# Optimization experiments

Measured on AMD Instinct MI355X. Metric: run time of the kernel, lower is better.

Reference implementation:

```python
import jax, jax.numpy as jnp
import numpy as np

B, S, H, NH = 4, 1024, 1024, 16
DH = H // NH  # 64


def setup_inputs() -> dict:
    key = jax.random.key(0)
    ks = jax.random.split(key, 12)
    f = lambda i, shape: jax.random.normal(ks[i], shape, jnp.float32) * 0.02
    inp = {
        "v": f(0, (B, S, H)),
        "k": f(1, (B, S, H)),
        "q": f(2, (B, S, H)),
        "s": f(3, (B, S, H)),
    }
    # padding-style key mask: last quarter of positions masked (True = masked)
    inp["mask"] = jnp.broadcast_to((jnp.arange(S) >= (3 * S) // 4)[None, None, None, :], (B, 1, 1, S))
    # weights stored as [in, out] so y = x @ W + b (== torch Linear with W = weight.T)
    for i, n in enumerate(["v", "k", "q", "m", "c", "ac"]):
        inp["W" + n] = f(4 + i, (H, H))
        inp["b" + n] = jnp.zeros((H,), jnp.float32)
    inp["Wcc"] = f(10, (H, 1)); inp["bcc"] = jnp.zeros((1,), jnp.float32)
    inp["Wcp"] = f(11, (H, 1)); inp["bcp"] = jnp.zeros((1,), jnp.float32)
    return inp


def reference(v, k, q, s, mask, Wv, bv, Wk, bk, Wq, bq, Wm, bm, Wc, bc, Wac, bac, Wcc, bcc, Wcp, bcp):
    # --- context gating path ---
    g_k = jnp.mean(s, axis=1, keepdims=True) @ Wac + bac          # [B,1,H]  (AdaptiveAvgPool2d((1,None)) + lin_ac)
    merge_p = (s @ Wc + bc) + (g_k @ Wcc + bcc)                   # [B,S,H] + [B,1,1]
    context_p = jax.nn.sigmoid(merge_p)                            # [B,S,H]
    context_gp = jax.nn.sigmoid(context_p @ Wcp + bcp)            # [B,S,1]

    # --- multi-head attention (dropout is identity in eval mode) ---
    def heads(x, W, b):
        return (x @ W + b).reshape(B, S, NH, DH).transpose(0, 2, 1, 3)  # [B,NH,S,DH]

    qh, kh, vh = heads(q, Wq, bq), heads(k, Wk, bk), heads(v, Wv, bv)
    scores = jnp.einsum("bhqd,bhkd->bhqk", qh, kh) / jnp.sqrt(jnp.float32(DH))
    scores = jnp.where(mask, jnp.float32(-1e9), scores)
    att = jax.nn.softmax(scores, axis=-1)
    atted = jnp.einsum("bhqk,bhkd->bhqd", att, vh)
    atted = atted.transpose(0, 2, 1, 3).reshape(B, S, H)
    atted = atted @ Wm + bm                                        # linear_merge
    return context_gp * atted + atted
```

## Files before the change

### kernel.cpp

```cpp
#include <hip/hip_runtime.h>
#include <stdint.h>

#define BB 4
#define SS 1024
#define HH 1024
#define NHEAD 16
#define DHEAD 64

typedef __attribute__((ext_vector_type(8))) short bf16x8;
typedef __attribute__((ext_vector_type(4))) float f32x4;

__device__ __forceinline__ unsigned short f2bf(float f) {
    union { float f; unsigned int u; } v; v.f = f;
    unsigned int r = v.u + 0x7fffu + ((v.u >> 16) & 1u);
    return (unsigned short)(r >> 16);
}
__device__ __forceinline__ float bf2f(unsigned short u) {
    union { float f; unsigned int u; } v; v.u = ((unsigned int)u) << 16;
    return v.f;
}

typedef const __attribute__((address_space(1))) unsigned int* gas_ptr;
typedef __attribute__((address_space(3))) unsigned int* las_ptr;
__device__ __forceinline__ void g2l16(const void* g, void* l) {
    __builtin_amdgcn_global_load_lds((gas_ptr)g, (las_ptr)l, 16, 0, 0);
}

__device__ __forceinline__ int aslot(int row, int c) {
    return row * 64 + ((c ^ (row & 7)) * 8);
}
#define AS_ROW(l) ((l) >> 3)
#define AS_COL(l) (((((l) & 7) ^ ((l) >> 3))) * 8)

__global__ __launch_bounds__(256) void k_prep(
    const float* __restrict__ W0, const float* __restrict__ W1,
    const float* __restrict__ W2, const float* __restrict__ W3,
    const float* __restrict__ W4,
    unsigned short* __restrict__ T0, unsigned short* __restrict__ T1,
    unsigned short* __restrict__ T2, unsigned short* __restrict__ T3,
    unsigned short* __restrict__ T4,
    const float* __restrict__ v, const float* __restrict__ k,
    const float* __restrict__ q, const float* __restrict__ s,
    unsigned short* __restrict__ Av, unsigned short* __restrict__ Ak,
    unsigned short* __restrict__ Aq, unsigned short* __restrict__ Ac,
    float* __restrict__ mpart,
    const float* __restrict__ Wac, const float* __restrict__ Wcc,
    float* __restrict__ u)
{
    int bid = blockIdx.x;
    int tid = threadIdx.x;
    if (bid < 1280) {
        int w = bid >> 8, rem = bid & 255;
        int kt = rem & 15, nt = rem >> 4;
        const float* W; unsigned short* T;
        switch (w) {
            case 0: W = W0; T = T0; break;
            case 1: W = W1; T = T1; break;
            case 2: W = W2; T = T2; break;
            case 3: W = W3; T = T3; break;
            default: W = W4; T = T4; break;
        }
        float scl = (w == 2) ? 0.125f : 1.0f;
        __shared__ unsigned short t[64][68];
        int k0 = kt * 64, n0 = nt * 64;
        int rb = tid >> 4;
        int c4 = (tid & 15) * 4;
#pragma unroll
        for (int i = 0; i < 4; i++) {
            int r = rb + i * 16;
            float4 wv = *(const float4*)&W[(size_t)(k0 + r) * HH + n0 + c4];
            t[c4 + 0][r] = f2bf(wv.x * scl);
            t[c4 + 1][r] = f2bf(wv.y * scl);
            t[c4 + 2][r] = f2bf(wv.z * scl);
            t[c4 + 3][r] = f2bf(wv.w * scl);
        }
        __syncthreads();
#pragma unroll
        for (int i = 0; i < 4; i++) {
            int r = rb + i * 16;
            ushort4 o;
            o.x = t[r][c4 + 0]; o.y = t[r][c4 + 1]; o.z = t[r][c4 + 2]; o.w = t[r][c4 + 3];
            *(ushort4*)&T[(size_t)(n0 + r) * HH + k0 + c4] = o;
        }
    } else if (bid < 9472) {
        int idx = bid - 1280;
        int tno = idx >> 11, blk = idx & 2047;
        const float* src; unsigned short* dst;
        switch (tno) {
            case 0: src = v; dst = Av; break;
            case 1: src = k; dst = Ak; break;
            case 2: src = q; dst = Aq; break;
            default: src = s; dst = Ac; break;
        }
        size_t i0 = ((size_t)blk * 256 + tid) * 8;
        float4 a = *(const float4*)&src[i0];
        float4 b = *(const float4*)&src[i0 + 4];
        bf16x8 o;
        o[0] = (short)f2bf(a.x); o[1] = (short)f2bf(a.y); o[2] = (short)f2bf(a.z); o[3] = (short)f2bf(a.w);
        o[4] = (short)f2bf(b.x); o[5] = (short)f2bf(b.y); o[6] = (short)f2bf(b.z); o[7] = (short)f2bf(b.w);
        *(bf16x8*)&dst[i0] = o;
    } else if (bid < 9728) {
        int idx = bid - 9472;
        int hc = idx & 3, b = (idx >> 2) & 3, g = idx >> 4;
        int h = hc * 256 + tid;
        const float* p = s + (size_t)b * SS * HH + (size_t)g * 64 * HH + h;
        float acc = 0.f;
        for (int i = 0; i < 64; i++) acc += p[(size_t)i * HH];
        mpart[(size_t)(b * 16 + g) * HH + h] = acc;
    } else {
        int idx = bid - 9728;
        int row = idx * 8 + (tid >> 5);
        int l32 = tid & 31;
        const float* wr = Wac + (size_t)row * HH;
        float acc = 0.f;
#pragma unroll
        for (int e = 0; e < 32; e++) {
            int h = l32 + e * 32;
            acc += wr[h] * Wcc[h];
        }
#pragma unroll
        for (int m = 1; m <= 16; m <<= 1) acc += __shfl_xor(acc, m, 64);
        if (l32 == 0) u[row] = acc;
    }
}

__global__ __launch_bounds__(256) void k_gemm4(
    const unsigned short* A0, const unsigned short* A1, const unsigned short* A2, const unsigned short* A3,
    const unsigned short* B0, const unsigned short* B1, const unsigned short* B2, const unsigned short* B3,
    const float* b0, const float* b1, const float* b2, const float* b3,
    unsigned short* D0, unsigned short* D1, unsigned short* D2, unsigned short* D3,
    const float* __restrict__ mpart, const float* __restrict__ u,
    const float* __restrict__ bac, const float* __restrict__ Wcc,
    const float* __restrict__ bcc)
{
    __shared__ unsigned short As[128 * 64];
    __shared__ unsigned short Bs[128 * 64];
    int f = blockIdx.x;
    int xcd = f & 7, j = f >> 3;
    int mp = xcd * 4 + (j >> 5);
    int z = (j >> 3) & 3;
    int n = j & 7;
    const unsigned short* A; const unsigned short* Bt; const float* bias; unsigned short* D; int mode; float bsc = 1.f;
    switch (z) {
        case 0: A = A0; Bt = B0; bias = b0; D = D0; mode = 3; break;
        case 1: A = A1; Bt = B1; bias = b1; D = D1; mode = 0; break;
        case 2: A = A2; Bt = B2; bias = b2; D = D2; mode = 0; bsc = 0.125f; break;
        default: A = A3; Bt = B3; bias = b3; D = D3; mode = 1; break;
    }
    int gm = mp * 128, gn = n * 128;
    int tid = threadIdx.x;
    int lane = tid & 63, wave = tid >> 6;
    int wm = (wave >> 1) * 64, wn = (wave & 1) * 64;
    int quad = lane >> 4, mcol = lane & 15;
    int lrow = lane >> 3;
    int gcol = ((lane & 7) ^ lrow) * 8;

    f32x4 acc[4][4];
#pragma unroll
    for (int i = 0; i < 4; i++)
#pragma unroll
        for (int jj = 0; jj < 4; jj++) acc[i][jj] = (f32x4){0.f, 0.f, 0.f, 0.f};

    for (int kk = 0; kk < 1024; kk += 64) {
#pragma unroll
        for (int i = 0; i < 4; i++) {
            int r0 = (wave * 4 + i) * 8;
            g2l16(&A[(size_t)(gm + r0 + lrow) * 1024 + kk + gcol], &As[r0 * 64]);
            g2l16(&Bt[(size_t)(gn + r0 + lrow) * 1024 + kk + gcol], &Bs[r0 * 64]);
        }
        __syncthreads();
#pragma unroll
        for (int kh = 0; kh < 2; kh++) {
            bf16x8 a[4], b[4];
#pragma unroll
            for (int i = 0; i < 4; i++) {
                int row = wm + i * 16 + mcol;
                int ch = (kh * 4 + quad) ^ (mcol & 7);
                a[i] = *(bf16x8*)&As[row * 64 + ch * 8];
            }
#pragma unroll
            for (int jj = 0; jj < 4; jj++) {
                int row = wn + jj * 16 + mcol;
                int ch = (kh * 4 + quad) ^ (mcol & 7);
                b[jj] = *(bf16x8*)&Bs[row * 64 + ch * 8];
            }
#pragma unroll
            for (int i = 0; i < 4; i++)
#pragma unroll
                for (int jj = 0; jj < 4; jj++)
                    acc[i][jj] = __builtin_amdgcn_mfma_f32_16x16x32_bf16(a[i], b[jj], acc[i][jj], 0, 0, 0);
        }
        __syncthreads();
    }

    float ccv = 0.f;
    if (mode == 1) {
        int b_ = gm >> 10;
        float sb = 0.f;
#pragma unroll
        for (int jj2 = 0; jj2 < 4; jj2++) {
            int h = tid + jj2 * 256;
            float cs = 0.f;
#pragma unroll
            for (int g = 0; g < 16; g++) cs += mpart[(size_t)(b_ * 16 + g) * HH + h];
            sb += cs * u[h] + bac[h] * Wcc[h] * 1024.0f;
        }
        float* red = (float*)As;
        red[tid] = sb; __syncthreads();
        for (int st = 128; st; st >>= 1) { if (tid < st) red[tid] += red[tid + st]; __syncthreads(); }
        ccv = red[0] * (1.0f / 1024.0f) + bcc[0];
    }
#pragma unroll
    for (int i = 0; i < 4; i++) {
        int row0 = gm + wm + i * 16 + quad * 4;
#pragma unroll
        for (int jj = 0; jj < 4; jj++) {
            int col = gn + wn + jj * 16 + mcol;
            float bv = bias[col] * bsc;
            if (mode == 3) {
                int b_ = row0 >> 10, tok0 = row0 & 1023;
                int h = col >> 6, d = col & 63;
                ushort4 o;
                o.x = f2bf(acc[i][jj][0] + bv);
                o.y = f2bf(acc[i][jj][1] + bv);
                o.z = f2bf(acc[i][jj][2] + bv);
                o.w = f2bf(acc[i][jj][3] + bv);
                *(ushort4*)&((unsigned short*)D)[((size_t)(b_ * 16 + h) * 64 + d) * 1024 + tok0] = o;
            } else {
#pragma unroll
                for (int r = 0; r < 4; r++) {
                    float vv = acc[i][jj][r] + bv;
                    int rr = row0 + r;
                    if (mode == 0) {
                        D[(size_t)rr * 1024 + col] = f2bf(vv);
                    } else {
                        vv = vv + ccv;
                        vv = 1.f / (1.f + __expf(-vv));
                        D[(size_t)rr * 1024 + col] = f2bf(vv);
                    }
                }
            }
        }
    }
}

__global__ __launch_bounds__(512) void k_gemmf(
    const unsigned short* __restrict__ A, const unsigned short* __restrict__ Bt,
    const float* __restrict__ bias, float* __restrict__ D, const float* __restrict__ gp)
{
    __shared__ unsigned short As[128 * 64];
    __shared__ unsigned short Bs[128 * 64];
    int f = blockIdx.x;
    int xcd = f & 7, j = f >> 3;
    int mp = xcd * 4 + (j >> 3);
    int n = j & 7;
    int gm = mp * 128, gn = n * 128;
    int tid = threadIdx.x;
    int lane = tid & 63, wave = tid >> 6;
    int wm = (wave >> 2) * 64, wn = (wave & 3) * 32;
    int quad = lane >> 4, mcol = lane & 15;
    int lrow = lane >> 3;
    int gcol = ((lane & 7) ^ lrow) * 8;

    f32x4 acc[4][2];
#pragma unroll
    for (int i = 0; i < 4; i++)
#pragma unroll
        for (int jj = 0; jj < 2; jj++) acc[i][jj] = (f32x4){0.f, 0.f, 0.f, 0.f};

    for (int kk = 0; kk < 1024; kk += 64) {
#pragma unroll
        for (int i = 0; i < 2; i++) {
            int r0 = (wave * 2 + i) * 8;
            g2l16(&A[(size_t)(gm + r0 + lrow) * 1024 + kk + gcol], &As[r0 * 64]);
            g2l16(&Bt[(size_t)(gn + r0 + lrow) * 1024 + kk + gcol], &Bs[r0 * 64]);
        }
        __syncthreads();
#pragma unroll
        for (int kh = 0; kh < 2; kh++) {
            bf16x8 a[4], b[2];
#pragma unroll
            for (int i = 0; i < 4; i++) {
                int row = wm + i * 16 + mcol;
                int ch = (kh * 4 + quad) ^ (mcol & 7);
                a[i] = *(bf16x8*)&As[row * 64 + ch * 8];
            }
#pragma unroll
            for (int jj = 0; jj < 2; jj++) {
                int row = wn + jj * 16 + mcol;
                int ch = (kh * 4 + quad) ^ (mcol & 7);
                b[jj] = *(bf16x8*)&Bs[row * 64 + ch * 8];
            }
#pragma unroll
            for (int i = 0; i < 4; i++)
#pragma unroll
                for (int jj = 0; jj < 2; jj++)
                    acc[i][jj] = __builtin_amdgcn_mfma_f32_16x16x32_bf16(a[i], b[jj], acc[i][jj], 0, 0, 0);
        }
        __syncthreads();
    }

#pragma unroll
    for (int i = 0; i < 4; i++) {
        int row0 = gm + wm + i * 16 + quad * 4;
#pragma unroll
        for (int jj = 0; jj < 2; jj++) {
            int col = gn + wn + jj * 16 + mcol;
            float bv = bias[col];
#pragma unroll
            for (int r = 0; r < 4; r++) {
                int rr = row0 + r;
                D[(size_t)rr * 1024 + col] = (acc[i][jj][r] + bv) * (1.f + gp[rr]);
            }
        }
    }
}

__global__ __launch_bounds__(256) void k_attnctx(
    const unsigned short* __restrict__ Pq,
    const unsigned short* __restrict__ Pk,
    const unsigned short* __restrict__ Pvt,
    unsigned short* __restrict__ atted,
    const unsigned short* __restrict__ Pc,
    const float* __restrict__ Wcp, const float* __restrict__ bcp,
    float* __restrict__ gp)
{
    int bid = blockIdx.x;
    int tid = threadIdx.x;
    int lane = tid & 63, wave = tid >> 6;

    if (bid >= 1024) {
        int rowbase = (bid - 1024) * 16 + wave * 4;
        float w[16];
#pragma unroll
        for (int e = 0; e < 4; e++) {
            float4 wv = *(const float4*)&Wcp[lane * 16 + e * 4];
            w[e * 4 + 0] = wv.x; w[e * 4 + 1] = wv.y; w[e * 4 + 2] = wv.z; w[e * 4 + 3] = wv.w;
        }
        float bcpv = bcp[0];
#pragma unroll
        for (int r = 0; r < 4; r++) {
            int row = rowbase + r;
            bf16x8 u0 = *(const bf16x8*)&Pc[(size_t)row * HH + lane * 16];
            bf16x8 u1 = *(const bf16x8*)&Pc[(size_t)row * HH + lane * 16 + 8];
            float sum = 0.f;
#pragma unroll
            for (int e = 0; e < 8; e++) sum += bf2f((unsigned short)u0[e]) * w[e];
#pragma unroll
            for (int e = 0; e < 8; e++) sum += bf2f((unsigned short)u1[e]) * w[8 + e];
#pragma unroll
            for (int m = 1; m <= 32; m <<= 1) sum += __shfl_xor(sum, m, 64);
            if (lane == 0) gp[row] = 1.f / (1.f + __expf(-(sum + bcpv)));
        }
        return;
    }

    __shared__ unsigned short Qs[64 * 64];
    __shared__ unsigned short Ks[2][64 * 64];
    __shared__ unsigned short Vt[2][64 * 64];
    __shared__ unsigned short Ps[64 * 76];

    int qt = bid & 15;
    int bh = bid >> 4;
    int b = bh >> 4, h = bh & 15;
    int quad = lane >> 4, mcol = lane & 15;
    int srow = AS_ROW(lane), scol = AS_COL(lane);

    size_t base_q = ((size_t)b * SS + qt * 64) * HH + h * 64;
    size_t base_vt = (size_t)(b * 16 + h) * 64 * 1024;

    {
        int r0 = wave * 16;
        g2l16(&Pq[base_q + (size_t)(r0 + srow) * HH + scol], &Qs[r0 * 64]);
        g2l16(&Pq[base_q + (size_t)(r0 + 8 + srow) * HH + scol], &Qs[(r0 + 8) * 64]);
        size_t base_k = (size_t)b * SS * HH + h * 64;
        g2l16(&Pk[base_k + (size_t)(r0 + srow) * HH + scol], &Ks[0][r0 * 64]);
        g2l16(&Pk[base_k + (size_t)(r0 + 8 + srow) * HH + scol], &Ks[0][(r0 + 8) * 64]);
        g2l16(&Pvt[base_vt + (size_t)(r0 + srow) * 1024 + scol], &Vt[0][r0 * 64]);
        g2l16(&Pvt[base_vt + (size_t)(r0 + 8 + srow) * 1024 + scol], &Vt[0][(r0 + 8) * 64]);
    }
    __syncthreads();
    int qrow = wave * 16 + mcol;
    bf16x8 bq0 = *(bf16x8*)&Qs[aslot(qrow, quad)];
    bf16x8 bq1 = *(bf16x8*)&Qs[aslot(qrow, quad + 4)];

    float lsum = 0.f;
    f32x4 acc_o[4];
#pragma unroll
    for (int dg = 0; dg < 4; dg++) acc_o[dg] = (f32x4){0.f, 0.f, 0.f, 0.f};

    for (int kt = 0; kt < 12; kt++) {
        int cur = kt & 1;
        if (kt < 11) {
            int r0 = wave * 16;
            size_t base_k = ((size_t)b * SS + (kt + 1) * 64) * HH + h * 64;
            g2l16(&Pk[base_k + (size_t)(r0 + srow) * HH + scol], &Ks[cur ^ 1][r0 * 64]);
            g2l16(&Pk[base_k + (size_t)(r0 + 8 + srow) * HH + scol], &Ks[cur ^ 1][(r0 + 8) * 64]);
            g2l16(&Pvt[base_vt + (size_t)(r0 + srow) * 1024 + (kt + 1) * 64 + scol], &Vt[cur ^ 1][r0 * 64]);
            g2l16(&Pvt[base_vt + (size_t)(r0 + 8 + srow) * 1024 + (kt + 1) * 64 + scol], &Vt[cur ^ 1][(r0 + 8) * 64]);
        }

#pragma unroll
        for (int kg = 0; kg < 4; kg++) {
            int krow = kg * 16 + mcol;
            bf16x8 aK0 = *(bf16x8*)&Ks[cur][aslot(krow, quad)];
            bf16x8 aK1 = *(bf16x8*)&Ks[cur][aslot(krow, quad + 4)];
            f32x4 st = (f32x4){0.f, 0.f, 0.f, 0.f};
            st = __builtin_amdgcn_mfma_f32_16x16x32_bf16(aK0, bq0, st, 0, 0, 0);
            st = __builtin_amdgcn_mfma_f32_16x16x32_bf16(aK1, bq1, st, 0, 0, 0);
            float p0 = __expf(st[0]), p1 = __expf(st[1]), p2 = __expf(st[2]), p3 = __expf(st[3]);
            lsum += (p0 + p1) + (p2 + p3);
            ushort4 o; o.x = f2bf(p0); o.y = f2bf(p1); o.z = f2bf(p2); o.w = f2bf(p3);
            *(ushort4*)&Ps[(wave * 16 + mcol) * 76 + kg * 16 + quad * 4] = o;
        }
        asm volatile("s_waitcnt lgkmcnt(0)" ::: "memory");
        bf16x8 ap0 = *(bf16x8*)&Ps[(wave * 16 + mcol) * 76 + quad * 8];
        bf16x8 ap1 = *(bf16x8*)&Ps[(wave * 16 + mcol) * 76 + 32 + quad * 8];
#pragma unroll
        for (int dg = 0; dg < 4; dg++) {
            int vrow = dg * 16 + mcol;
            bf16x8 bV0 = *(bf16x8*)&Vt[cur][aslot(vrow, quad)];
            bf16x8 bV1 = *(bf16x8*)&Vt[cur][aslot(vrow, quad + 4)];
            acc_o[dg] = __builtin_amdgcn_mfma_f32_16x16x32_bf16(ap0, bV0, acc_o[dg], 0, 0, 0);
            acc_o[dg] = __builtin_amdgcn_mfma_f32_16x16x32_bf16(ap1, bV1, acc_o[dg], 0, 0, 0);
        }
        __syncthreads();
    }
    lsum += __shfl_xor(lsum, 16, 64);
    lsum += __shfl_xor(lsum, 32, 64);
    float linv_all = 1.f / lsum;
    float liv[4];
#pragma unroll
    for (int r = 0; r < 4; r++) liv[r] = __shfl(linv_all, quad * 4 + r, 64);

    size_t obase = ((size_t)b * SS + qt * 64 + wave * 16 + quad * 4) * HH + h * 64;
#pragma unroll
    for (int dg = 0; dg < 4; dg++)
#pragma unroll
        for (int r = 0; r < 4; r++)
            atted[obase + (size_t)r * HH + dg * 16 + mcol] = f2bf(acc_o[dg][r] * liv[r]);
}

extern "C" void kernel_launch(void* const* d_in, const int* in_sizes, int n_in,
                              void* d_out, int out_size, void* d_ws, size_t ws_size,
                              hipStream_t stream)
{
    (void)in_sizes; (void)n_in; (void)out_size; (void)ws_size;
    const float* v   = (const float*)d_in[0];
    const float* k   = (const float*)d_in[1];
    const float* q   = (const float*)d_in[2];
    const float* s   = (const float*)d_in[3];
    const float* Wv  = (const float*)d_in[5];  const float* bv  = (const float*)d_in[6];
    const float* Wk  = (const float*)d_in[7];  const float* bk  = (const float*)d_in[8];
    const float* Wq  = (const float*)d_in[9];  const float* bq  = (const float*)d_in[10];
    const float* Wm  = (const float*)d_in[11]; const float* bm  = (const float*)d_in[12];
    const float* Wc  = (const float*)d_in[13]; const float* bc  = (const float*)d_in[14];
    const float* Wac = (const float*)d_in[15]; const float* bac = (const float*)d_in[16];
    const float* Wcc = (const float*)d_in[17]; const float* bcc = (const float*)d_in[18];
    const float* Wcp = (const float*)d_in[19]; const float* bcp = (const float*)d_in[20];

    char* ws = (char*)d_ws;
    const size_t MB = 1024 * 1024;
    unsigned short* Wtv   = (unsigned short*)(ws + 0 * MB);
    unsigned short* Wtk   = (unsigned short*)(ws + 2 * MB);
    unsigned short* Wtq   = (unsigned short*)(ws + 4 * MB);
    unsigned short* Wtc   = (unsigned short*)(ws + 6 * MB);
    unsigned short* Wtm   = (unsigned short*)(ws + 8 * MB);
    unsigned short* Av    = (unsigned short*)(ws + 10 * MB);
    unsigned short* Ak    = (unsigned short*)(ws + 18 * MB);
    unsigned short* Aq    = (unsigned short*)(ws + 26 * MB);
    unsigned short* Ac    = (unsigned short*)(ws + 34 * MB);
    unsigned short* Pk    = (unsigned short*)(ws + 42 * MB);
    unsigned short* Pq    = (unsigned short*)(ws + 50 * MB);
    unsigned short* Pvt   = (unsigned short*)(ws + 58 * MB);
    unsigned short* Pc    = (unsigned short*)(ws + 66 * MB);
    unsigned short* atted = Av;
    float* mpart = (float*)(ws + 74 * MB);
    float* u     = (float*)(ws + 74 * MB + 262144);
    float* gp    = (float*)(ws + 74 * MB + 262144 + 8192);
    float* out = (float*)d_out;

    k_prep<<<9856, 256, 0, stream>>>(Wv, Wk, Wq, Wc, Wm, Wtv, Wtk, Wtq, Wtc, Wtm,
                                     v, k, q, s, Av, Ak, Aq, Ac,
                                     mpart, Wac, Wcc, u);
    k_gemm4<<<1024, 256, 0, stream>>>(Av, Ak, Aq, Ac,
                                      Wtv, Wtk, Wtq, Wtc,
                                      bv, bk, bq, bc,
                                      Pvt, Pk, Pq, Pc,
                                      mpart, u, bac, Wcc, bcc);
    k_attnctx<<<1280, 256, 0, stream>>>(Pq, Pk, Pvt, atted, Pc, Wcp, bcp, gp);
    k_gemmf<<<256, 512, 0, stream>>>(atted, Wtm, bm, out, gp);
}
```

Measured before the change: 267.8 us.

## Double-buffer GEMM staging, fuse s conversion with mean, split attention MFMA chains

The projection GEMM now double-buffers its A/B tiles in LDS, prefetching the next k-step while the current one computes, using explicit waitcnt, barriers and setprio. Its block-to-XCD mapping changes so each XCD handles a single projection. The prep kernel fuses the bf16 conversion of s with the column-sum used for the mean, so s is read once instead of twice. The attention kernel splits the score and PV MFMA accumulation into independent chains to shorten dependency stalls. Doubling LDS per block and adding launch_bounds(256,2) may limit occupancy.

```diff
diff --git a/kernel.cpp b/kernel.cpp
--- a/kernel.cpp
+++ b/kernel.cpp
@@ -82,15 +82,14 @@
             o.x = t[r][c4 + 0]; o.y = t[r][c4 + 1]; o.z = t[r][c4 + 2]; o.w = t[r][c4 + 3];
             *(ushort4*)&T[(size_t)(n0 + r) * HH + k0 + c4] = o;
         }
-    } else if (bid < 9472) {
+    } else if (bid < 7424) {
         int idx = bid - 1280;
         int tno = idx >> 11, blk = idx & 2047;
         const float* src; unsigned short* dst;
         switch (tno) {
             case 0: src = v; dst = Av; break;
             case 1: src = k; dst = Ak; break;
-            case 2: src = q; dst = Aq; break;
-            default: src = s; dst = Ac; break;
+            default: src = q; dst = Aq; break;
         }
         size_t i0 = ((size_t)blk * 256 + tid) * 8;
         float4 a = *(const float4*)&src[i0];
@@ -99,16 +98,24 @@
         o[0] = (short)f2bf(a.x); o[1] = (short)f2bf(a.y); o[2] = (short)f2bf(a.z); o[3] = (short)f2bf(a.w);
         o[4] = (short)f2bf(b.x); o[5] = (short)f2bf(b.y); o[6] = (short)f2bf(b.z); o[7] = (short)f2bf(b.w);
         *(bf16x8*)&dst[i0] = o;
-    } else if (bid < 9728) {
-        int idx = bid - 9472;
-        int hc = idx & 3, b = (idx >> 2) & 3, g = idx >> 4;
-        int h = hc * 256 + tid;
-        const float* p = s + (size_t)b * SS * HH + (size_t)g * 64 * HH + h;
-        float acc = 0.f;
-        for (int i = 0; i < 64; i++) acc += p[(size_t)i * HH];
-        mpart[(size_t)(b * 16 + g) * HH + h] = acc;
+    } else if (bid < 7552) {
+        int idx = bid - 7424;
+        int hc = idx & 1, g = (idx >> 1) & 15, b = idx >> 5;
+        int h0 = hc * 512 + tid * 2;
+        const float* ps = s + ((size_t)b * SS + g * 64) * HH + h0;
+        unsigned short* pd = Ac + ((size_t)b * SS + g * 64) * HH + h0;
+        float s0 = 0.f, s1 = 0.f;
+#pragma unroll 4
+        for (int r = 0; r < 64; r++) {
+            float2 xv = *(const float2*)&ps[(size_t)r * HH];
+            s0 += xv.x; s1 += xv.y;
+            ushort2 o; o.x = f2bf(xv.x); o.y = f2bf(xv.y);
+            *(ushort2*)&pd[(size_t)r * HH] = o;
+        }
+        float2 ms; ms.x = s0; ms.y = s1;
+        *(float2*)&mpart[(size_t)(b * 16 + g) * HH + h0] = ms;
     } else {
-        int idx = bid - 9728;
+        int idx = bid - 7552;
         int row = idx * 8 + (tid >> 5);
         int l32 = tid & 31;
         const float* wr = Wac + (size_t)row * HH;
@@ -124,7 +131,7 @@
     }
 }
 
-__global__ __launch_bounds__(256) void k_gemm4(
+__global__ __launch_bounds__(256, 2) void k_gemm4(
     const unsigned short* A0, const unsigned short* A1, const unsigned short* A2, const unsigned short* A3,
     const unsigned short* B0, const unsigned short* B1, const unsigned short* B2, const unsigned short* B3,
     const float* b0, const float* b1, const float* b2, const float* b3,
@@ -133,14 +140,15 @@
     const float* __restrict__ bac, const float* __restrict__ Wcc,
     const float* __restrict__ bcc)
 {
-    __shared__ unsigned short As[128 * 64];
-    __shared__ unsigned short Bs[128 * 64];
+    __shared__ unsigned short As[2][128 * 64];
+    __shared__ unsigned short Bs[2][128 * 64];
     int f = blockIdx.x;
     int xcd = f & 7, j = f >> 3;
-    int mp = xcd * 4 + (j >> 5);
-    int z = (j >> 3) & 3;
+    int z = xcd >> 1;
+    int mp = (xcd & 1) * 16 + (j >> 3);
     int n = j & 7;
-    const unsigned short* A; const unsigned short* Bt; const float* bias; unsigned short* D; int mode; float bsc = 1.f;
+    const unsigned short* A; const unsigned short* Bt; const float* bias;
+    unsigned short* D; int mode; float bsc = 1.f;
     switch (z) {
         case 0: A = A0; Bt = B0; bias = b0; D = D0; mode = 3; break;
         case 1: A = A1; Bt = B1; bias = b1; D = D1; mode = 0; break;
@@ -161,37 +169,69 @@
 #pragma unroll
         for (int jj = 0; jj < 4; jj++) acc[i][jj] = (f32x4){0.f, 0.f, 0.f, 0.f};
 
-    for (int kk = 0; kk < 1024; kk += 64) {
-#pragma unroll
-        for (int i = 0; i < 4; i++) {
-            int r0 = (wave * 4 + i) * 8;
-            g2l16(&A[(size_t)(gm + r0 + lrow) * 1024 + kk + gcol], &As[r0 * 64]);
-            g2l16(&Bt[(size_t)(gn + r0 + lrow) * 1024 + kk + gcol], &Bs[r0 * 64]);
-        }
-        __syncthreads();
+#define STG(Mp, g0, kkc, lb) do {                                                              \
+        int r0_ = wave * 32;                                                                   \
+        g2l16(&Mp[(size_t)((g0) + r0_ + 0  + lrow) * 1024 + (kkc) + gcol], &(lb)[(r0_ + 0)  * 64]); \
+        g2l16(&Mp[(size_t)((g0) + r0_ + 8  + lrow) * 1024 + (kkc) + gcol], &(lb)[(r0_ + 8)  * 64]); \
+        g2l16(&Mp[(size_t)((g0) + r0_ + 16 + lrow) * 1024 + (kkc) + gcol], &(lb)[(r0_ + 16) * 64]); \
+        g2l16(&Mp[(size_t)((g0) + r0_ + 24 + lrow) * 1024 + (kkc) + gcol], &(lb)[(r0_ + 24) * 64]); \
+    } while (0)
+
+    STG(A,  gm, 0, As[0]);
+    STG(Bt, gn, 0, Bs[0]);
+
+    for (int g = 0; g < 16; ++g) {
+        int cur = g & 1, nxt = cur ^ 1;
+        int k1 = (g + 1) * 64;
+        bf16x8 a[4][2], b[4][2];
+
+        if (g + 1 < 16) {
+            STG(A, gm, k1, As[nxt]);
+            asm volatile("s_waitcnt vmcnt(4)" ::: "memory");
+        } else {
+            asm volatile("s_waitcnt vmcnt(0)" ::: "memory");
+        }
+        __builtin_amdgcn_s_barrier();
+        __builtin_amdgcn_sched_barrier(0);
 #pragma unroll
         for (int kh = 0; kh < 2; kh++) {
-            bf16x8 a[4], b[4];
 #pragma unroll
             for (int i = 0; i < 4; i++) {
                 int row = wm + i * 16 + mcol;
-                int ch = (kh * 4 + quad) ^ (mcol & 7);
-                a[i] = *(bf16x8*)&As[row * 64 + ch * 8];
+                a[i][kh] = *(const bf16x8*)&As[cur][row * 64 + (((kh * 4 + quad) ^ (mcol & 7)) * 8)];
             }
 #pragma unroll
             for (int jj = 0; jj < 4; jj++) {
                 int row = wn + jj * 16 + mcol;
-                int ch = (kh * 4 + quad) ^ (mcol & 7);
-                b[jj] = *(bf16x8*)&Bs[row * 64 + ch * 8];
+                b[jj][kh] = *(const bf16x8*)&Bs[cur][row * 64 + (((kh * 4 + quad) ^ (mcol & 7)) * 8)];
             }
+        }
+        __builtin_amdgcn_s_setprio(1);
+#pragma unroll
+        for (int kh = 0; kh < 2; kh++)
 #pragma unroll
             for (int i = 0; i < 4; i++)
 #pragma unroll
-                for (int jj = 0; jj < 4; jj++)
-                    acc[i][jj] = __builtin_amdgcn_mfma_f32_16x16x32_bf16(a[i], b[jj], acc[i][jj], 0, 0, 0);
-        }
-        __syncthreads();
-    }
+                for (int jj = 0; jj < 2; jj++)
+                    acc[i][jj] = __builtin_amdgcn_mfma_f32_16x16x32_bf16(a[i][kh], b[jj][kh], acc[i][jj], 0, 0, 0);
+        __builtin_amdgcn_s_setprio(0);
+
+        if (g + 1 < 16) STG(Bt, gn, k1, Bs[nxt]);
+        __builtin_amdgcn_s_setprio(1);
+#pragma unroll
+        for (int kh = 0; kh < 2; kh++)
+#pragma unroll
+            for (int i = 0; i < 4; i++)
+#pragma unroll
+                for (int jj = 2; jj < 4; jj++)
+                    acc[i][jj] = __builtin_amdgcn_mfma_f32_16x16x32_bf16(a[i][kh], b[jj][kh], acc[i][jj], 0, 0, 0);
+        __builtin_amdgcn_s_setprio(0);
+        asm volatile("s_waitcnt lgkmcnt(0)" ::: "memory");
+        __builtin_amdgcn_sched_barrier(0);
+        __builtin_amdgcn_s_barrier();
+        __builtin_amdgcn_sched_barrier(0);
+    }
+#undef STG
 
     float ccv = 0.f;
     if (mode == 1) {
@@ -202,12 +242,12 @@
             int h = tid + jj2 * 256;
             float cs = 0.f;
 #pragma unroll
-            for (int g = 0; g < 16; g++) cs += mpart[(size_t)(b_ * 16 + g) * HH + h];
+            for (int gg = 0; gg < 16; gg++) cs += mpart[(size_t)(b_ * 16 + gg) * HH + h];
             sb += cs * u[h] + bac[h] * Wcc[h] * 1024.0f;
         }
-        float* red = (float*)As;
+        float* red = (float*)&As[0][0];
         red[tid] = sb; __syncthreads();
-        for (int st = 128; st; st >>= 1) { if (tid < st) red[tid] += red[tid + st]; __syncthreads(); }
+        for (int st2 = 128; st2; st2 >>= 1) { if (tid < st2) red[tid] += red[tid + st2]; __syncthreads(); }
         ccv = red[0] * (1.0f / 1024.0f) + bcc[0];
     }
 #pragma unroll
@@ -385,9 +425,13 @@
     bf16x8 bq1 = *(bf16x8*)&Qs[aslot(qrow, quad + 4)];
 
     float lsum = 0.f;
-    f32x4 acc_o[4];
-#pragma unroll
-    for (int dg = 0; dg < 4; dg++) acc_o[dg] = (f32x4){0.f, 0.f, 0.f, 0.f};
+    f32x4 accE[4], accO[4];
+#pragma unroll
+    for (int dg = 0; dg < 4; dg++) {
+        accE[dg] = (f32x4){0.f, 0.f, 0.f, 0.f};
+        accO[dg] = (f32x4){0.f, 0.f, 0.f, 0.f};
+    }
+    const f32x4 z4 = (f32x4){0.f, 0.f, 0.f, 0.f};
 
     for (int kt = 0; kt < 12; kt++) {
         int cur = kt & 1;
@@ -405,9 +449,9 @@
             int krow = kg * 16 + mcol;
             bf16x8 aK0 = *(bf16x8*)&Ks[cur][aslot(krow, quad)];
             bf16x8 aK1 = *(bf16x8*)&Ks[cur][aslot(krow, quad + 4)];
-            f32x4 st = (f32x4){0.f, 0.f, 0.f, 0.f};
-            st = __builtin_amdgcn_mfma_f32_16x16x32_bf16(aK0, bq0, st, 0, 0, 0);
-            st = __builtin_amdgcn_mfma_f32_16x16x32_bf16(aK1, bq1, st, 0, 0, 0);
+            f32x4 st0 = __builtin_amdgcn_mfma_f32_16x16x32_bf16(aK0, bq0, z4, 0, 0, 0);
+            f32x4 st1 = __builtin_amdgcn_mfma_f32_16x16x32_bf16(aK1, bq1, z4, 0, 0, 0);
+            f32x4 st = st0 + st1;
             float p0 = __expf(st[0]), p1 = __expf(st[1]), p2 = __expf(st[2]), p3 = __expf(st[3]);
             lsum += (p0 + p1) + (p2 + p3);
             ushort4 o; o.x = f2bf(p0); o.y = f2bf(p1); o.z = f2bf(p2); o.w = f2bf(p3);
@@ -416,13 +460,17 @@
         asm volatile("s_waitcnt lgkmcnt(0)" ::: "memory");
         bf16x8 ap0 = *(bf16x8*)&Ps[(wave * 16 + mcol) * 76 + quad * 8];
         bf16x8 ap1 = *(bf16x8*)&Ps[(wave * 16 + mcol) * 76 + 32 + quad * 8];
+        bf16x8 bV0[4], bV1[4];
 #pragma unroll
         for (int dg = 0; dg < 4; dg++) {
             int vrow = dg * 16 + mcol;
-            bf16x8 bV0 = *(bf16x8*)&Vt[cur][aslot(vrow, quad)];
-            bf16x8 bV1 = *(bf16x8*)&Vt[cur][aslot(vrow, quad + 4)];
-            acc_o[dg] = __builtin_amdgcn_mfma_f32_16x16x32_bf16(ap0, bV0, acc_o[dg], 0, 0, 0);
-            acc_o[dg] = __builtin_amdgcn_mfma_f32_16x16x32_bf16(ap1, bV1, acc_o[dg], 0, 0, 0);
+            bV0[dg] = *(bf16x8*)&Vt[cur][aslot(vrow, quad)];
+            bV1[dg] = *(bf16x8*)&Vt[cur][aslot(vrow, quad + 4)];
+        }
+#pragma unroll
+        for (int dg = 0; dg < 4; dg++) {
+            accE[dg] = __builtin_amdgcn_mfma_f32_16x16x32_bf16(ap0, bV0[dg], accE[dg], 0, 0, 0);
+            accO[dg] = __builtin_amdgcn_mfma_f32_16x16x32_bf16(ap1, bV1[dg], accO[dg], 0, 0, 0);
         }
         __syncthreads();
     }
@@ -435,10 +483,12 @@
 
     size_t obase = ((size_t)b * SS + qt * 64 + wave * 16 + quad * 4) * HH + h * 64;
 #pragma unroll
-    for (int dg = 0; dg < 4; dg++)
+    for (int dg = 0; dg < 4; dg++) {
+        f32x4 o4 = accE[dg] + accO[dg];
 #pragma unroll
         for (int r = 0; r < 4; r++)
-            atted[obase + (size_t)r * HH + dg * 16 + mcol] = f2bf(acc_o[dg][r] * liv[r]);
+            atted[obase + (size_t)r * HH + dg * 16 + mcol] = f2bf(o4[r] * liv[r]);
+    }
 }
 
 extern "C" void kernel_launch(void* const* d_in, const int* in_sizes, int n_in,
@@ -480,7 +530,7 @@
     float* gp    = (float*)(ws + 74 * MB + 262144 + 8192);
     float* out = (float*)d_out;
 
-    k_prep<<<9856, 256, 0, stream>>>(Wv, Wk, Wq, Wc, Wm, Wtv, Wtk, Wtq, Wtc, Wtm,
+    k_prep<<<7680, 256, 0, stream>>>(Wv, Wk, Wq, Wc, Wm, Wtv, Wtk, Wtq, Wtc, Wtm,
                                      v, k, q, s, Av, Ak, Aq, Ac,
                                      mpart, Wac, Wcc, u);
     k_gemm4<<<1024, 256, 0, stream>>>(Av, Ak, Aq, Ac,
```

Result: no change. 271.6 us (+1.4%).
